# Optimization experiments

Measured on AMD Instinct MI355X. Metric: run time of the kernel, lower is better.

The kernel has to match this reference:

```python
import jax, jax.numpy as jnp
import numpy as np
from jax import lax

# ---- dims / config (see init_kwargs) ----
M_IMG, N_PCD, C = 1008, 1024, 256     # coarse img nodes (24*32+12*16+6*8), coarse pcd nodes, feat dim
NI_F, NP_F = 76800, 30000             # fine img pixels (240*320), fine pcd points
KI, KP = 64, 64                       # knn patch sizes
NUM_CORR, TOPK = 256, 3               # coarse matching params
COARSE_THR, FINE_THR = 0.0, 0.0       # similarity thresholds (lowered for random data)


def _norm(x):
    return x / (jnp.linalg.norm(x, axis=-1, keepdims=True) + 1e-8)


def setup_inputs() -> dict:
    key = jax.random.key(0)
    ks = jax.random.split(key, 7)
    return {
        "img_feats_c": _norm(jax.random.normal(ks[0], (M_IMG, C), jnp.float32)),
        "pcd_feats_c": _norm(jax.random.normal(ks[1], (N_PCD, C), jnp.float32)),
        "img_feats_f": _norm(jax.random.normal(ks[2], (NI_F, C), jnp.float32)),
        "pcd_feats_f": _norm(jax.random.normal(ks[3], (NP_F, C), jnp.float32)),
        "img_node_masks": jnp.ones((M_IMG,), bool),
        "pcd_node_masks": jnp.ones((N_PCD,), bool),
        "img_node_knn_indices": jax.random.randint(ks[4], (M_IMG, KI), 0, NI_F),
        "pcd_node_knn_indices": jax.random.randint(ks[5], (N_PCD, KP), 0, NP_F),
        "pcd_node_knn_masks": jax.random.uniform(ks[6], (N_PCD, KP)) > 0.1,
    }


def _coarse_match(img_feats_c, pcd_feats_c, img_masks, pcd_masks):
    # SuperPointMatchingMutualTopk: cosine sim + mutual top-k + global top NUM_CORR
    sim = img_feats_c @ pcd_feats_c.T                              # [M, N] (feats normalized)
    valid = img_masks[:, None] & pcd_masks[None, :]
    sim_m = jnp.where(valid, sim, -jnp.inf)
    row_kth = lax.top_k(sim_m, TOPK)[0][:, -1:]                    # kth-largest per row [M,1]
    col_kth = lax.top_k(sim_m.T, TOPK)[0][:, -1:].T                # kth-largest per col [1,N]
    mutual = (sim_m >= row_kth) & (sim_m >= col_kth) & (sim_m > COARSE_THR)
    flat = jnp.where(mutual, sim_m, -jnp.inf).ravel()
    vals, flat_idx = lax.top_k(flat, NUM_CORR)                     # fixed-size selection
    img_idx = flat_idx // N_PCD
    pcd_idx = flat_idx % N_PCD
    corr_valid = jnp.isfinite(vals)
    return img_idx, pcd_idx, corr_valid


def reference(img_feats_c, pcd_feats_c, img_feats_f, pcd_feats_f,
              img_node_masks, pcd_node_masks,
              img_node_knn_indices, pcd_node_knn_indices, pcd_node_knn_masks):
    # ---- coarse matching ----
    img_idx, pcd_idx, corr_valid = _coarse_match(
        img_feats_c, pcd_feats_c, img_node_masks, pcd_node_masks)

    # ---- fine matching: knn gather + pairwise cosine + mutual top-1 ----
    pcd_padded = jnp.concatenate([pcd_feats_f, jnp.zeros_like(pcd_feats_f[:1])], axis=0)
    img_knn_idx = img_node_knn_indices[img_idx]                    # [Ci, KI]
    pcd_knn_idx = pcd_node_knn_indices[pcd_idx]                    # [Ci, KP]
    pcd_knn_msk = pcd_node_knn_masks[pcd_idx]                      # [Ci, KP]
    img_knn_feats = img_feats_f[img_knn_idx]                       # [Ci, KI, C]
    pcd_knn_feats = pcd_padded[pcd_knn_idx]                        # [Ci, KP, C]

    sim = jnp.einsum('bic,bjc->bij', img_knn_feats, pcd_knn_feats) # [Ci, KI, KP]
    m3 = corr_valid[:, None, None] & pcd_knn_msk[:, None, :]
    sim = jnp.where(m3, sim, -jnp.inf)

    row_best = jnp.argmax(sim, axis=2)                             # [Ci, KI]
    row_val = jnp.max(sim, axis=2)
    col_best = jnp.argmax(sim, axis=1)                             # [Ci, KP]
    back = jnp.take_along_axis(col_best, row_best, axis=1)         # [Ci, KI]
    sel = (back == jnp.arange(KI)[None, :]) & jnp.isfinite(row_val) & (row_val > FINE_THR)

    img_corr = img_knn_idx.reshape(-1)                             # [Ci*KI]
    pcd_corr = jnp.take_along_axis(pcd_knn_idx, row_best, axis=1).reshape(-1)
    sel = sel.reshape(-1)
    # sentinel for unselected pairs -> sorts last
    img_corr = jnp.where(sel, img_corr, NI_F)
    pcd_corr = jnp.where(sel, pcd_corr, NP_F)

    # ---- dedup (torch.unique on img*Npf+pcd) via lexsort + first-occurrence mask ----
    order = jnp.lexsort((pcd_corr, img_corr))
    ic, pc = img_corr[order], pcd_corr[order]
    first = jnp.concatenate([jnp.array([True]),
                             (ic[1:] != ic[:-1]) | (pc[1:] != pc[:-1])])
    valid = first & (ic < NI_F)

    ic_s = jnp.clip(ic, 0, NI_F - 1)
    pc_s = jnp.clip(pc, 0, NP_F - 1)
    corr_scores = jnp.sum(img_feats_f[ic_s] * pcd_feats_f[pc_s], axis=1)
    corr_scores = corr_scores * valid.astype(corr_scores.dtype)    # masked scores [Ci*KI]
    return corr_scores
```

## Files before the change

### kernel.cpp

```cpp
#include <hip/hip_runtime.h>

#define M_IMG 1008
#define N_PCD 1024
#define CDIM  256
#define NI_F  76800
#define NP_F  30000
#define KI    64
#define KP    64
#define NUM_CORR 256
#define NPAIR (NUM_CORR * KI)
#define KEY_MOD 30001u
#define NCHUNK 21
#define SORT_N 4096
#define NEG_INF (-__builtin_inff())

__device__ __forceinline__ bool mask_val(const void* p, int i, int is_u8) {
    return is_u8 ? (((const unsigned char*)p)[i] != 0)
                 : (((const int*)p)[i] != 0);
}

__device__ __forceinline__ void top3_insert(float v, float& t0, float& t1, float& t2) {
    if (v > t0) { t2 = t1; t1 = t0; t0 = v; }
    else if (v > t1) { t2 = t1; t1 = v; }
    else if (v > t2) { t2 = v; }
}

__device__ __forceinline__ void top3_merge(float a0, float a1, float a2,
                                           float b0, float b1, float b2,
                                           float& x0, float& x1, float& x2) {
    if (a0 >= b0) {
        x0 = a0;
        if (a1 >= b0) { x1 = a1; x2 = (a2 >= b0) ? a2 : b0; }
        else          { x1 = b0; x2 = (a1 >= b1) ? a1 : b1; }
    } else {
        x0 = b0;
        if (b1 >= a0) { x1 = b1; x2 = (b2 >= a0) ? b2 : a0; }
        else          { x1 = a0; x2 = (b1 >= a1) ? b1 : a1; }
    }
}

__device__ __forceinline__ void t3i_insert(float v, int i,
                                           float& v0, int& i0,
                                           float& v1, int& i1,
                                           float& v2, int& i2) {
    if (v > v0) { v2 = v1; i2 = i1; v1 = v0; i1 = i0; v0 = v; i0 = i; }
    else if (v > v1) { v2 = v1; i2 = i1; v1 = v; i1 = i; }
    else if (v > v2) { v2 = v; i2 = i; }
}

__global__ void coarse_sim_kernel(const float* __restrict__ A,
                                  const float* __restrict__ B,
                                  const void* __restrict__ maskA,
                                  const void* __restrict__ maskB,
                                  const unsigned int* __restrict__ mskw,
                                  float* __restrict__ sim,
                                  float* __restrict__ out0,
                                  unsigned int* __restrict__ cnt,
                                  int* __restrict__ nk) {
    __shared__ __align__(16) float s_a[32][36];
    __shared__ __align__(16) float s_b[32][68];
    const int m0 = blockIdx.y * 32, n0 = blockIdx.x * 64;
    const int tid = threadIdx.x;
    const int tx = tid & 15, ty = tid >> 4;
    const int c_lane = tid & 31;
    const int r_base = tid >> 5;

    const int bid = blockIdx.y * 16 + blockIdx.x;
    if (tid < 32) out0[bid * 32 + tid] = 0.f;
    if (tid >= 32 && tid < 64) cnt[bid * 32 + (tid - 32)] = 0u;
    if (bid == 0 && tid == 64) *nk = 0;

    const bool hit = (mskw[tid] & 0xFFFFFF00u) != 0u;

    const float* pa[4];
    const float* pb[8];
#pragma unroll
    for (int k = 0; k < 4; k++) {
        int m = m0 + r_base + 8 * k;
        pa[k] = A + (size_t)(m < M_IMG ? m : 0) * CDIM + c_lane;
    }
#pragma unroll
    for (int k = 0; k < 8; k++)
        pb[k] = B + (size_t)(n0 + r_base + 8 * k) * CDIM + c_lane;

    float ra[4], rb[8];
#pragma unroll
    for (int k = 0; k < 4; k++) ra[k] = pa[k][0];
#pragma unroll
    for (int k = 0; k < 8; k++) rb[k] = pb[k][0];
#pragma unroll
    for (int k = 0; k < 4; k++) s_a[c_lane][r_base + 8 * k] = ra[k];
#pragma unroll
    for (int k = 0; k < 8; k++) s_b[c_lane][r_base + 8 * k] = rb[k];
    __syncthreads();

    float acc[2][4];
#pragma unroll
    for (int r = 0; r < 2; r++)
#pragma unroll
        for (int j = 0; j < 4; j++) acc[r][j] = 0.f;

    for (int cit = 0; cit < 8; cit++) {
        if (cit < 7) {
            const int cc = (cit + 1) * 32;
#pragma unroll
            for (int k = 0; k < 4; k++) ra[k] = pa[k][cc];
#pragma unroll
            for (int k = 0; k < 8; k++) rb[k] = pb[k][cc];
        }
#pragma unroll 8
        for (int c = 0; c < 32; c++) {
            float2 av = *(const float2*)&s_a[c][ty * 2];
            float4 bv = *(const float4*)&s_b[c][tx * 4];
            float ar[2] = {av.x, av.y};
            float br[4] = {bv.x, bv.y, bv.z, bv.w};
#pragma unroll
            for (int r = 0; r < 2; r++)
#pragma unroll
                for (int j = 0; j < 4; j++) acc[r][j] += ar[r] * br[j];
        }
        __syncthreads();
        if (cit < 7) {
#pragma unroll
            for (int k = 0; k < 4; k++) s_a[c_lane][r_base + 8 * k] = ra[k];
#pragma unroll
            for (int k = 0; k < 8; k++) s_b[c_lane][r_base + 8 * k] = rb[k];
            __syncthreads();
        }
    }

    const int is_u8 = __syncthreads_or(hit ? 1 : 0);
#pragma unroll
    for (int r = 0; r < 2; r++) {
        int m = m0 + ty * 2 + r;
        if (m < M_IMG) {
            bool ma = mask_val(maskA, m, is_u8);
#pragma unroll
            for (int j = 0; j < 4; j++) {
                int n = n0 + tx * 4 + j;
                bool ok = ma && mask_val(maskB, n, is_u8);
                sim[m * N_PCD + n] = ok ? acc[r][j] : NEG_INF;
            }
        }
    }
}

__global__ void kth_kernel(const float* __restrict__ sim,
                           float* __restrict__ rowv3,
                           int* __restrict__ rowi3,
                           float* __restrict__ colp) {
    __shared__ float sv[256][3];
    __shared__ int   si[256][3];
    const int tid = threadIdx.x;
    if (blockIdx.x < M_IMG) {
        const float* r = sim + (size_t)blockIdx.x * N_PCD;
        float v0 = NEG_INF, v1 = NEG_INF, v2 = NEG_INF;
        int i0 = 0, i1 = 0, i2 = 0;
#pragma unroll
        for (int e = 0; e < 4; e++) {
            int c = e * 256 + tid;
            t3i_insert(r[c], c, v0, i0, v1, i1, v2, i2);
        }
        sv[tid][0] = v0; sv[tid][1] = v1; sv[tid][2] = v2;
        si[tid][0] = i0; si[tid][1] = i1; si[tid][2] = i2;
        __syncthreads();
        for (int s = 128; s > 0; s >>= 1) {
            if (tid < s) {
                float a0 = sv[tid][0], a1 = sv[tid][1], a2 = sv[tid][2];
                int   j0 = si[tid][0], j1 = si[tid][1], j2 = si[tid][2];
#pragma unroll
                for (int k = 0; k < 3; k++)
                    t3i_insert(sv[tid + s][k], si[tid + s][k],
                               a0, j0, a1, j1, a2, j2);
                sv[tid][0] = a0; sv[tid][1] = a1; sv[tid][2] = a2;
                si[tid][0] = j0; si[tid][1] = j1; si[tid][2] = j2;
            }
            __syncthreads();
        }
        if (tid < 3) {
            rowv3[blockIdx.x * 3 + tid] = sv[0][tid];
            rowi3[blockIdx.x * 3 + tid] = si[0][tid];
        }
    } else {
        const int b = blockIdx.x - M_IMG;
        const int bx = b & 15, by = b >> 4;
        const int c = tid & 63, rr = tid >> 6;
        const int col = bx * 64 + c;
        const int r0 = by * 48;
        float t0 = NEG_INF, t1 = NEG_INF, t2 = NEG_INF;
#pragma unroll
        for (int k = 0; k < 12; k++) {
            float v = sim[(size_t)(r0 + rr + 4 * k) * N_PCD + col];
            top3_insert(v, t0, t1, t2);
        }
        sv[tid][0] = t0; sv[tid][1] = t1; sv[tid][2] = t2;
        __syncthreads();
        if (tid < 128) {
            float x0, x1, x2;
            top3_merge(sv[tid][0], sv[tid][1], sv[tid][2],
                       sv[tid + 128][0], sv[tid + 128][1], sv[tid + 128][2],
                       x0, x1, x2);
            sv[tid][0] = x0; sv[tid][1] = x1; sv[tid][2] = x2;
        }
        __syncthreads();
        if (tid < 64) {
            float x0, x1, x2;
            top3_merge(sv[tid][0], sv[tid][1], sv[tid][2],
                       sv[tid + 64][0], sv[tid + 64][1], sv[tid + 64][2],
                       x0, x1, x2);
            const int base = by * N_PCD + col;
            colp[base] = x0;
            colp[NCHUNK * N_PCD + base] = x1;
            colp[2 * NCHUNK * N_PCD + base] = x2;
        }
    }
}

__global__ __launch_bounds__(1024)
void merge_select_kernel(const float* __restrict__ colp,
                         const float* __restrict__ rowv3,
                         const int* __restrict__ rowi3,
                         int* __restrict__ sel_idx,
                         int* __restrict__ selK) {
    __shared__ float s_colk[N_PCD];
    __shared__ __align__(16) unsigned long long s_cand[SORT_N];
    __shared__ int s_cnt;
    const int tid = threadIdx.x;

    {
        float t0 = colp[tid];
        float t1 = colp[NCHUNK * N_PCD + tid];
        float t2 = colp[2 * NCHUNK * N_PCD + tid];
#pragma unroll 4
        for (int ch = 1; ch < NCHUNK; ch++) {
            float b0 = colp[ch * N_PCD + tid];
            float b1 = colp[NCHUNK * N_PCD + ch * N_PCD + tid];
            float b2 = colp[2 * NCHUNK * N_PCD + ch * N_PCD + tid];
            float x0, x1, x2;
            top3_merge(t0, t1, t2, b0, b1, b2, x0, x1, x2);
            t0 = x0; t1 = x1; t2 = x2;
        }
        s_colk[tid] = t2;
    }
    if (tid == 0) s_cnt = 0;
    for (int i = tid; i < SORT_N; i += 1024) s_cand[i] = ~0ULL;
    __syncthreads();

    for (int e = tid; e < M_IMG * 3; e += 1024) {
        float v = rowv3[e];
        int n = rowi3[e];
        if (v > 0.f && v >= s_colk[n]) {
            int m = e / 3;
            int g = m * N_PCD + n;
            unsigned int u = __float_as_uint(v);
            unsigned int mono = (u & 0x80000000u) ? ~u : (u | 0x80000000u);
            int pos = atomicAdd(&s_cnt, 1);
            s_cand[pos] = ((unsigned long long)(~mono) << 32) | (unsigned int)g;
        }
    }
    __syncthreads();
    int K = s_cnt;

    for (int k = 2; k <= SORT_N; k <<= 1) {
        for (int j = k >> 1; j > 0; j >>= 1) {
            for (int i = tid; i < SORT_N; i += 1024) {
                int ixj = i ^ j;
                if (ixj > i) {
                    bool up = ((i & k) == 0);
                    unsigned long long a = s_cand[i], b = s_cand[ixj];
                    if ((a > b) == up) { s_cand[i] = b; s_cand[ixj] = a; }
                }
            }
            __syncthreads();
        }
    }

    if (K > NUM_CORR) K = NUM_CORR;
    if (tid == 0) *selK = K;
    if (tid < K) sel_idx[tid] = (int)(s_cand[tid] & 0xFFFFFFFFu);
}

__global__ void fine_kernel(const float* __restrict__ img_f,
                            const float* __restrict__ pcd_f,
                            const int* __restrict__ img_knn,
                            const int* __restrict__ pcd_knn,
                            const void* __restrict__ pcd_msk,
                            const unsigned int* __restrict__ mskw,
                            const int* __restrict__ sel_idx,
                            const int* __restrict__ selK_ptr,
                            int* __restrict__ nk,
                            unsigned int* __restrict__ ckeys,
                            float* __restrict__ cscore) {
    const int ci = blockIdx.x, tid = threadIdx.x;
    if (ci >= *selK_ptr) return;
    __shared__ int s_ik[KI], s_pk[KP];
    __shared__ unsigned char s_mk[KP];
    __shared__ __align__(16) float s_a[32][68];
    __shared__ __align__(16) float s_b[32][68];
    __shared__ float s_sim[64][65];
    __shared__ int s_rb[64], s_cb[64];
    __shared__ float s_rv[64];

    const bool hit = (mskw[tid & 255] & 0xFFFFFF00u) != 0u;
    int flat = sel_idx[ci];
    int gi = flat >> 10, pi = flat & 1023;
    if (tid < 64) {
        s_ik[tid] = img_knn[gi * KI + tid];
        s_pk[tid] = pcd_knn[pi * KP + tid];
    }
    const int is_u8 = __syncthreads_or(hit ? 1 : 0);
    if (tid < 64)
        s_mk[tid] = mask_val(pcd_msk, pi * KP + tid, is_u8) ? 1 : 0;

    const int tx = tid & 15, tyy = tid >> 4;
    const int c_lane = tid & 31;
    const int r_base = tid >> 5;

    const float* pa[4];
    const float* pb[4];
#pragma unroll
    for (int k = 0; k < 4; k++) {
        pa[k] = img_f + (size_t)s_ik[r_base + 16 * k] * CDIM + c_lane;
        pb[k] = pcd_f + (size_t)s_pk[r_base + 16 * k] * CDIM + c_lane;
    }

    float ra[4], rb[4];
#pragma unroll
    for (int k = 0; k < 4; k++) { ra[k] = pa[k][0]; rb[k] = pb[k][0]; }
#pragma unroll
    for (int k = 0; k < 4; k++) {
        s_a[c_lane][r_base + 16 * k] = ra[k];
        s_b[c_lane][r_base + 16 * k] = rb[k];
    }
    __syncthreads();

    float acc[2][4];
#pragma unroll
    for (int r = 0; r < 2; r++)
#pragma unroll
        for (int j = 0; j < 4; j++) acc[r][j] = 0.f;

    for (int cit = 0; cit < 8; cit++) {
        if (cit < 7) {
            const int cc = (cit + 1) * 32;
#pragma unroll
            for (int k = 0; k < 4; k++) { ra[k] = pa[k][cc]; rb[k] = pb[k][cc]; }
        }
#pragma unroll 8
        for (int c = 0; c < 32; c++) {
            float2 av = *(const float2*)&s_a[c][tyy * 2];
            float4 bv = *(const float4*)&s_b[c][tx * 4];
            float ar[2] = {av.x, av.y};
            float br[4] = {bv.x, bv.y, bv.z, bv.w};
#pragma unroll
            for (int r = 0; r < 2; r++)
#pragma unroll
                for (int j = 0; j < 4; j++) acc[r][j] += ar[r] * br[j];
        }
        __syncthreads();
        if (cit < 7) {
#pragma unroll
            for (int k = 0; k < 4; k++) {
                s_a[c_lane][r_base + 16 * k] = ra[k];
                s_b[c_lane][r_base + 16 * k] = rb[k];
            }
            __syncthreads();
        }
    }
#pragma unroll
    for (int r = 0; r < 2; r++) {
        int row = tyy * 2 + r;
#pragma unroll
        for (int j = 0; j < 4; j++) {
            int kp = tx * 4 + j;
            s_sim[row][kp] = (s_mk[kp] != 0) ? acc[r][j] : NEG_INF;
        }
    }
    __syncthreads();

    if (tid < 64) {
        float best = NEG_INF; int bi = 0;
        for (int kp = 0; kp < 64; kp++) {
            float v = s_sim[tid][kp];
            if (v > best) { best = v; bi = kp; }
        }
        s_rb[tid] = bi; s_rv[tid] = best;
    } else if (tid < 128) {
        int kp = tid - 64;
        float best = NEG_INF; int bi = 0;
        for (int k2 = 0; k2 < 64; k2++) {
            float v = s_sim[k2][kp];
            if (v > best) { best = v; bi = k2; }
        }
        s_cb[kp] = bi;
    }
    __syncthreads();

    if (tid < 64) {
        int rb2 = s_rb[tid];
        float rv = s_rv[tid];
        if ((s_cb[rb2] == tid) && (rv > 0.f)) {
            int ik = s_ik[tid];
            int pk = s_pk[rb2];
            unsigned int key = (unsigned int)ik * KEY_MOD + (unsigned int)pk;
            const float4* a = (const float4*)(img_f + (size_t)ik * CDIM);
            const float4* b = (const float4*)(pcd_f + (size_t)pk * CDIM);
            float s = 0.f;
#pragma unroll 8
            for (int c = 0; c < CDIM / 4; c++) {
                float4 x = a[c], y = b[c];
                s += x.x * y.x + x.y * y.y + x.z * y.z + x.w * y.w;
            }
            int pos = atomicAdd(nk, 1);
            ckeys[pos] = key;
            cscore[pos] = s;
        }
    }
}

__global__ void rank_count_kernel(const unsigned int* __restrict__ ckeys,
                                  const int* __restrict__ nk,
                                  unsigned int* __restrict__ cnt) {
    const int K = *nk;
    const int bi = blockIdx.x, bj = blockIdx.y;
    if (bi * 256 >= K || bj * 256 >= K) return;
    __shared__ unsigned int s_k[256];
    const int tid = threadIdx.x;
    const int i = bi * 256 + tid;
    const unsigned int myKey = (i < K) ? ckeys[i] : 0xFFFFFFFFu;
    const int j = bj * 256 + tid;
    s_k[tid] = (j < K) ? ckeys[j] : 0xFFFFFFFFu;
    __syncthreads();

    unsigned int less = 0, eqb = 0;
    if (bj < bi) {
#pragma unroll 8
        for (int t = 0; t < 256; t++) {
            unsigned int k = s_k[t];
            less += (k < myKey);
            eqb += (k == myKey);
        }
    } else if (bj == bi) {
#pragma unroll 8
        for (int t = 0; t < 256; t++) {
            unsigned int k = s_k[t];
            less += (k < myKey);
            eqb += (k == myKey) & (t < tid);
        }
    } else {
#pragma unroll 8
        for (int t = 0; t < 256; t++) {
            unsigned int k = s_k[t];
            less += (k < myKey);
        }
    }
    unsigned int v = (less << 16) | eqb;
    if (i < K && v) atomicAdd(&cnt[i], v);
}

__global__ void rank_out_kernel(const unsigned int* __restrict__ cnt,
                                const float* __restrict__ cscore,
                                const int* __restrict__ nk,
                                float* __restrict__ out) {
    const int K = *nk;
    const int i = blockIdx.x * 256 + threadIdx.x;
    if (i >= K) return;
    const unsigned int v = cnt[i];
    if ((v & 0xFFFFu) == 0)
        out[v >> 16] = cscore[i];
}

extern "C" void kernel_launch(void* const* d_in, const int* in_sizes, int n_in,
                              void* d_out, int out_size, void* d_ws, size_t ws_size,
                              hipStream_t stream) {
    const float* img_c = (const float*)d_in[0];
    const float* pcd_c = (const float*)d_in[1];
    const float* img_f = (const float*)d_in[2];
    const float* pcd_f = (const float*)d_in[3];
    const void* img_mask = d_in[4];
    const void* pcd_mask = d_in[5];
    const int* img_knn = (const int*)d_in[6];
    const int* pcd_knn = (const int*)d_in[7];
    const void* pcd_knn_msk = d_in[8];
    float* out = (float*)d_out;

    char* w = (char*)d_ws;
    size_t off = 0;
    float* sim = (float*)(w + off);            off += (size_t)M_IMG * N_PCD * 4;
    float* colp = (float*)(w + off);           off += 3 * NCHUNK * N_PCD * 4;
    float* rowv3 = (float*)(w + off);          off += M_IMG * 3 * 4;
    int* rowi3 = (int*)(w + off);              off += M_IMG * 3 * 4;
    int* sel_idx = (int*)(w + off);            off += NUM_CORR * 4;
    int* selK = (int*)(w + off);               off += 4;
    int* nk = (int*)(w + off);                 off += 4;
    unsigned int* ckeys = (unsigned int*)(w + off); off += NPAIR * 4;
    float* cscore = (float*)(w + off);         off += NPAIR * 4;
    unsigned int* cnt = (unsigned int*)(w + off);   off += NPAIR * 4;

    const unsigned int* mskw = (const unsigned int*)pcd_knn_msk;

    coarse_sim_kernel<<<dim3(16, 32), 256, 0, stream>>>(
        img_c, pcd_c, img_mask, pcd_mask, mskw, sim, out, cnt, nk);
    kth_kernel<<<M_IMG + 16 * NCHUNK, 256, 0, stream>>>(sim, rowv3, rowi3, colp);
    merge_select_kernel<<<1, 1024, 0, stream>>>(colp, rowv3, rowi3, sel_idx, selK);
    fine_kernel<<<NUM_CORR, 512, 0, stream>>>(img_f, pcd_f, img_knn, pcd_knn,
                                              pcd_knn_msk, mskw, sel_idx, selK,
                                              nk, ckeys, cscore);
    rank_count_kernel<<<dim3(64, 64), 256, 0, stream>>>(ckeys, nk, cnt);
    rank_out_kernel<<<64, 256, 0, stream>>>(cnt, cscore, nk, out);
}
```

Baseline: 282.6 us.

## Replace single-block bitonic sort with multi-block rank selection and full-column kth

The column top-3 pass now has each of 16 blocks scan all 1008 rows of its 64 columns directly, which removes the chunked partial buffer and its later merge. The single-block 4096-element bitonic sort is replaced by a prefix-scan compaction of mutual candidates followed by a rank-by-counting selection spread over 12 blocks, each block ranking 256 candidates. The intent is to cut the long serial sort and merge stage. In exchange, the column pass has much less parallelism (16 blocks each doing long strided loops), and every select block redundantly rebuilds the compacted candidate list.

```diff
diff --git a/kernel.cpp b/kernel.cpp
--- a/kernel.cpp
+++ b/kernel.cpp
@@ -10,8 +10,7 @@
 #define NUM_CORR 256
 #define NPAIR (NUM_CORR * KI)
 #define KEY_MOD 30001u
-#define NCHUNK 21
-#define SORT_N 4096
+#define NCAND (M_IMG * 3)
 #define NEG_INF (-__builtin_inff())
 
 __device__ __forceinline__ bool mask_val(const void* p, int i, int is_u8) {
@@ -148,7 +147,7 @@
 __global__ void kth_kernel(const float* __restrict__ sim,
                            float* __restrict__ rowv3,
                            int* __restrict__ rowi3,
-                           float* __restrict__ colp) {
+                           float* __restrict__ col_kth) {
     __shared__ float sv[256][3];
     __shared__ int   si[256][3];
     const int tid = threadIdx.x;
@@ -183,16 +182,12 @@
         }
     } else {
         const int b = blockIdx.x - M_IMG;
-        const int bx = b & 15, by = b >> 4;
-        const int c = tid & 63, rr = tid >> 6;
-        const int col = bx * 64 + c;
-        const int r0 = by * 48;
+        const int col = b * 64 + (tid & 63);
+        const int rr = tid >> 6;
         float t0 = NEG_INF, t1 = NEG_INF, t2 = NEG_INF;
-#pragma unroll
-        for (int k = 0; k < 12; k++) {
-            float v = sim[(size_t)(r0 + rr + 4 * k) * N_PCD + col];
-            top3_insert(v, t0, t1, t2);
-        }
+#pragma unroll 4
+        for (int r = rr; r < M_IMG; r += 4)
+            top3_insert(sim[(size_t)r * N_PCD + col], t0, t1, t2);
         sv[tid][0] = t0; sv[tid][1] = t1; sv[tid][2] = t2;
         __syncthreads();
         if (tid < 128) {
@@ -208,76 +203,89 @@
             top3_merge(sv[tid][0], sv[tid][1], sv[tid][2],
                        sv[tid + 64][0], sv[tid + 64][1], sv[tid + 64][2],
                        x0, x1, x2);
-            const int base = by * N_PCD + col;
-            colp[base] = x0;
-            colp[NCHUNK * N_PCD + base] = x1;
-            colp[2 * NCHUNK * N_PCD + base] = x2;
+            col_kth[col] = x2;
         }
     }
 }
 
 __global__ __launch_bounds__(1024)
-void merge_select_kernel(const float* __restrict__ colp,
-                         const float* __restrict__ rowv3,
-                         const int* __restrict__ rowi3,
-                         int* __restrict__ sel_idx,
-                         int* __restrict__ selK) {
+void select_kernel(const float* __restrict__ rowv3,
+                   const int* __restrict__ rowi3,
+                   const float* __restrict__ col_kth,
+                   int* __restrict__ sel_idx,
+                   int* __restrict__ selK) {
     __shared__ float s_colk[N_PCD];
-    __shared__ __align__(16) unsigned long long s_cand[SORT_N];
-    __shared__ int s_cnt;
+    __shared__ __align__(16) unsigned long long s_key[NCAND];
+    __shared__ int s_part[1024];
+    __shared__ int s_wsum[16];
     const int tid = threadIdx.x;
-
-    {
-        float t0 = colp[tid];
-        float t1 = colp[NCHUNK * N_PCD + tid];
-        float t2 = colp[2 * NCHUNK * N_PCD + tid];
-#pragma unroll 4
-        for (int ch = 1; ch < NCHUNK; ch++) {
-            float b0 = colp[ch * N_PCD + tid];
-            float b1 = colp[NCHUNK * N_PCD + ch * N_PCD + tid];
-            float b2 = colp[2 * NCHUNK * N_PCD + ch * N_PCD + tid];
-            float x0, x1, x2;
-            top3_merge(t0, t1, t2, b0, b1, b2, x0, x1, x2);
-            t0 = x0; t1 = x1; t2 = x2;
-        }
-        s_colk[tid] = t2;
-    }
-    if (tid == 0) s_cnt = 0;
-    for (int i = tid; i < SORT_N; i += 1024) s_cand[i] = ~0ULL;
-    __syncthreads();
-
-    for (int e = tid; e < M_IMG * 3; e += 1024) {
-        float v = rowv3[e];
-        int n = rowi3[e];
-        if (v > 0.f && v >= s_colk[n]) {
-            int m = e / 3;
-            int g = m * N_PCD + n;
-            unsigned int u = __float_as_uint(v);
-            unsigned int mono = (u & 0x80000000u) ? ~u : (u | 0x80000000u);
-            int pos = atomicAdd(&s_cnt, 1);
-            s_cand[pos] = ((unsigned long long)(~mono) << 32) | (unsigned int)g;
-        }
-    }
-    __syncthreads();
-    int K = s_cnt;
-
-    for (int k = 2; k <= SORT_N; k <<= 1) {
-        for (int j = k >> 1; j > 0; j >>= 1) {
-            for (int i = tid; i < SORT_N; i += 1024) {
-                int ixj = i ^ j;
-                if (ixj > i) {
-                    bool up = ((i & k) == 0);
-                    unsigned long long a = s_cand[i], b = s_cand[ixj];
-                    if ((a > b) == up) { s_cand[i] = b; s_cand[ixj] = a; }
-                }
+    const int lane = tid & 63, w = tid >> 6;
+
+    s_colk[tid] = col_kth[tid];
+    __syncthreads();
+
+    unsigned long long k0 = 0, k1 = 0, k2 = 0;
+    int f0 = 0, f1 = 0, f2 = 0;
+    if (tid < M_IMG) {
+#pragma unroll
+        for (int s = 0; s < 3; s++) {
+            float v = rowv3[tid * 3 + s];
+            int n = rowi3[tid * 3 + s];
+            if (v > 0.f && v >= s_colk[n]) {
+                unsigned int u = __float_as_uint(v);
+                unsigned int mono = (u & 0x80000000u) ? ~u : (u | 0x80000000u);
+                unsigned long long key =
+                    ((unsigned long long)(~mono) << 32)
+                    | (unsigned int)(tid * N_PCD + n);
+                if (s == 0) { k0 = key; f0 = 1; }
+                else if (s == 1) { k1 = key; f1 = 1; }
+                else { k2 = key; f2 = 1; }
             }
-            __syncthreads();
-        }
-    }
-
-    if (K > NUM_CORR) K = NUM_CORR;
-    if (tid == 0) *selK = K;
-    if (tid < K) sel_idx[tid] = (int)(s_cand[tid] & 0xFFFFFFFFu);
+        }
+    }
+    const int c = f0 + f1 + f2;
+
+    int v = c;
+#pragma unroll
+    for (int d = 1; d < 64; d <<= 1) {
+        int o = __shfl_up(v, d);
+        if (lane >= d) v += o;
+    }
+    if (lane == 63) s_wsum[w] = v;
+    __syncthreads();
+    if (w == 0) {
+        int x = (lane < 16) ? s_wsum[lane] : 0;
+#pragma unroll
+        for (int d = 1; d < 16; d <<= 1) {
+            int o = __shfl_up(x, d);
+            if (lane >= d) x += o;
+        }
+        if (lane < 16) s_wsum[lane] = x;
+    }
+    __syncthreads();
+    const int K = s_wsum[15];
+    int pos = v - c + (w > 0 ? s_wsum[w - 1] : 0);
+
+    if (f0) s_key[pos++] = k0;
+    if (f1) s_key[pos++] = k1;
+    if (f2) s_key[pos++] = k2;
+    __syncthreads();
+
+    if (blockIdx.x == 0 && tid == 0) *selK = (K < NUM_CORR) ? K : NUM_CORR;
+
+    const int ii = tid & 255, q = tid >> 8;
+    const int i = blockIdx.x * 256 + ii;
+    const unsigned long long my = (i < K) ? s_key[i] : 0xFFFFFFFFFFFFFFFFull;
+    int less = 0;
+    for (int j = q; j < K; j += 4)
+        less += (s_key[j] < my);
+    s_part[tid] = less;
+    __syncthreads();
+    if (q == 0 && i < K) {
+        int rank = s_part[ii] + s_part[ii + 256] + s_part[ii + 512] + s_part[ii + 768];
+        if (rank < NUM_CORR)
+            sel_idx[rank] = (int)(s_key[i] & 0xFFFFFFFFull);
+    }
 }
 
 __global__ void fine_kernel(const float* __restrict__ img_f,
@@ -487,9 +495,9 @@
     char* w = (char*)d_ws;
     size_t off = 0;
     float* sim = (float*)(w + off);            off += (size_t)M_IMG * N_PCD * 4;
-    float* colp = (float*)(w + off);           off += 3 * NCHUNK * N_PCD * 4;
     float* rowv3 = (float*)(w + off);          off += M_IMG * 3 * 4;
     int* rowi3 = (int*)(w + off);              off += M_IMG * 3 * 4;
+    float* col_kth = (float*)(w + off);        off += N_PCD * 4;
     int* sel_idx = (int*)(w + off);            off += NUM_CORR * 4;
     int* selK = (int*)(w + off);               off += 4;
     int* nk = (int*)(w + off);                 off += 4;
@@ -501,8 +509,8 @@
 
     coarse_sim_kernel<<<dim3(16, 32), 256, 0, stream>>>(
         img_c, pcd_c, img_mask, pcd_mask, mskw, sim, out, cnt, nk);
-    kth_kernel<<<M_IMG + 16 * NCHUNK, 256, 0, stream>>>(sim, rowv3, rowi3, colp);
-    merge_select_kernel<<<1, 1024, 0, stream>>>(colp, rowv3, rowi3, sel_idx, selK);
+    kth_kernel<<<M_IMG + 16, 256, 0, stream>>>(sim, rowv3, rowi3, col_kth);
+    select_kernel<<<12, 1024, 0, stream>>>(rowv3, rowi3, col_kth, sel_idx, selK);
     fine_kernel<<<NUM_CORR, 512, 0, stream>>>(img_f, pcd_f, img_knn, pcd_knn,
                                               pcd_knn_msk, mskw, sel_idx, selK,
                                               nk, ckeys, cscore);
```

New measurement: 353.8 us. +25.2%, slower.
